# Performance work log

Hardware: AMD Instinct MI355X
Metric: run time of the kernel (lower is better)

## Reference

```python
import jax, jax.numpy as jnp
import numpy as np

B, N = 128, 65536
POS_FRAC = 0.02  # sparse positives, realistic for detection


def setup_inputs() -> dict:
    key = jax.random.key(0)
    k1, k2 = jax.random.split(key)
    pred = jax.random.normal(k1, (B, N), dtype=jnp.float32)
    label = (jax.random.uniform(k2, (B, N)) < POS_FRAC).astype(jnp.float32)
    return {"pred": pred, "label": label}


def _focal_loss_with_mask(pred, label, gamma=2.0, alpha=0.75, negative_ratio=3.0):
    # BCE with logits, elementwise: y*softplus(-x) + (1-y)*softplus(x)
    loss = label * jax.nn.softplus(-pred) + (1.0 - label) * jax.nn.softplus(pred)
    p = jax.nn.sigmoid(pred)
    p_t = label * p + (1.0 - label) * (1.0 - p)
    loss = loss * (1.0 - p_t) ** gamma
    loss = loss * (label * alpha + (1.0 - label) * (1.0 - alpha))

    fn_mask = (p < 0.5) & (label == 1.0)
    fp_mask = (p >= 0.5) & (label == 0.0)

    # --- hard negative mining (vectorized rank-based selection) ---
    pos_mask = label > 0
    num_pos = pos_mask.sum(axis=1, keepdims=True)              # [B,1]
    num_neg = jnp.floor(negative_ratio * num_pos).astype(jnp.int32)  # int() truncation as in torch
    loss_m = jnp.where(pos_mask, -jnp.inf, loss)               # positives sorted last
    order = jnp.argsort(-loss_m, axis=1)                       # descending sort indices
    ranks = jnp.argsort(order, axis=1)                         # rank of each element
    neg_mask = ranks < num_neg
    relevant = pos_mask | neg_mask

    w = alpha / (1.0 - alpha)
    loss = jnp.where(fn_mask | fp_mask, loss * w, loss)
    rm = relevant.astype(loss.dtype)
    return (loss * rm).sum() / rm.sum()


def reference(pred, label):
    return _focal_loss_with_mask(pred, label)
```

## Files before the change

### kernel.cpp

```cpp
#include <hip/hip_runtime.h>
#include <cstdint>
#include <cstddef>

constexpr int B_ROWS = 128;
constexpr int N_COLS = 65536;
constexpr int CAP    = 4096;

constexpr size_t OFF_HISTCNT = 0;
constexpr size_t OFF_CAND    = (size_t)1 << 20;
constexpr size_t OFF_MISC    = (size_t)3 << 20;
constexpr size_t MO_NUMPOS   = 0;
constexpr size_t MO_SPOS     = 512;
constexpr size_t MO_ROWS     = 1024;
constexpr size_t MO_ROWDEN   = 2048;
constexpr size_t MO_CANDBIN  = 2560;
constexpr size_t MO_R1       = 3072;
constexpr size_t MO_KARR     = 3584;
constexpr size_t MO_CANDCNT  = 4096;
constexpr size_t MO_SABOVE   = 4608;
constexpr size_t MO_AUTO64   = 5120;
constexpr size_t MISC_ZERO   = 6144;
constexpr size_t OFF_KEYS    = (size_t)4 << 20;

__device__ __forceinline__ unsigned key_from_pred(float x) {
  unsigned b = __float_as_uint(x);
  return (b & 0x80000000u) ? ~b : (b | 0x80000000u);
}
__device__ __forceinline__ float pred_from_key(unsigned k) {
  unsigned b = (k & 0x80000000u) ? (k ^ 0x80000000u) : ~k;
  return __uint_as_float(b);
}

__device__ __forceinline__ float neg_loss(float x) {
  float ax = fabsf(x);
  float e  = expf(-ax);
  float p  = (x >= 0.0f) ? 1.0f / (1.0f + e) : e / (1.0f + e);
  float sp = fmaxf(x, 0.0f) + log1pf(e);
  float f  = p;
  float l  = sp * f * f * 0.25f;
  return (p >= 0.5f) ? l * 3.0f : l;
}
__device__ __forceinline__ float pos_loss(float x) {
  float ax = fabsf(x);
  float e  = expf(-ax);
  float p  = (x >= 0.0f) ? 1.0f / (1.0f + e) : e / (1.0f + e);
  float sp = fmaxf(-x, 0.0f) + log1pf(e);
  float f  = 1.0f - p;
  float l  = sp * f * f * 0.75f;
  return (p < 0.5f) ? l * 3.0f : l;
}
__device__ __forceinline__ float loss_from_key(unsigned k) { return neg_loss(pred_from_key(k)); }

__device__ void suffix_scan(int* c, float* l, int M) {
  const int T = blockDim.x;
  const int i0 = threadIdx.x, i1 = threadIdx.x + T;
  for (int d = 1; d < M; d <<= 1) {
    int vi0 = 0, vi1 = 0; float vf0 = 0.0f, vf1 = 0.0f;
    const bool h0 = i0 < M, h1 = i1 < M;
    if (h0) { vi0 = c[i0] + ((i0 + d < M) ? c[i0 + d] : 0);
              vf0 = l[i0] + ((i0 + d < M) ? l[i0 + d] : 0.0f); }
    if (h1) { vi1 = c[i1] + ((i1 + d < M) ? c[i1 + d] : 0);
              vf1 = l[i1] + ((i1 + d < M) ? l[i1 + d] : 0.0f); }
    __syncthreads();
    if (h0) { c[i0] = vi0; l[i0] = vf0; }
    if (h1) { c[i1] = vi1; l[i1] = vf1; }
    __syncthreads();
  }
}
__device__ void suffix_scan_i(int* c, int M) {
  const int T = blockDim.x;
  const int i0 = threadIdx.x, i1 = threadIdx.x + T;
  for (int d = 1; d < M; d <<= 1) {
    int v0 = 0, v1 = 0;
    const bool h0 = i0 < M, h1 = i1 < M;
    if (h0) v0 = c[i0] + ((i0 + d < M) ? c[i0 + d] : 0);
    if (h1) v1 = c[i1] + ((i1 + d < M) ? c[i1 + d] : 0);
    __syncthreads();
    if (h0) c[i0] = v0;
    if (h1) c[i1] = v1;
    __syncthreads();
  }
}
__device__ int find_cut(const int* sc, int M, int r, int* ctrl) {
  __syncthreads();
  if (threadIdx.x == 0) *ctrl = -1;
  __syncthreads();
  int loc = -1;
  for (int i = threadIdx.x; i < M; i += blockDim.x)
    if (sc[i] >= r) loc = i;
  if (loc >= 0) atomicMax(ctrl, loc);
  __syncthreads();
  return *ctrl;
}

constexpr int K1_TPB = 256;
constexpr int K1_SEGS = 8;
constexpr int K1_SEG_ELEMS = N_COLS / K1_SEGS;
constexpr int K1_ITERS = K1_SEG_ELEMS / (K1_TPB * 4);

template <bool STORE_KEYS>
__global__ __launch_bounds__(K1_TPB)
void k1_hist(const float* __restrict__ pred, const float* __restrict__ label,
             int* __restrict__ histCnt, int* __restrict__ numPos, float* __restrict__ SPos,
             unsigned* __restrict__ keys)
{
  __shared__ int   hcnt[2048];
  __shared__ int   wnp[K1_TPB / 64];
  __shared__ float wsp[K1_TPB / 64];
  const int tid = threadIdx.x;
  for (int i = tid; i < 2048; i += K1_TPB) hcnt[i] = 0;
  __syncthreads();

  const int row = blockIdx.x / K1_SEGS;
  const int seg = blockIdx.x % K1_SEGS;
  const size_t base = (size_t)row * N_COLS + (size_t)seg * K1_SEG_ELEMS;
  const float4* p4 = reinterpret_cast<const float4*>(pred + base);
  const float4* l4 = reinterpret_cast<const float4*>(label + base);
  uint4* k4 = STORE_KEYS ? reinterpret_cast<uint4*>(keys + base) : nullptr;

  int npos = 0; float spos = 0.0f;
  for (int it = 0; it < K1_ITERS; ++it) {
    const int vi = it * K1_TPB + tid;
    const float4 pv = p4[vi];
    const float4 lv = l4[vi];
    const float xs[4] = {pv.x, pv.y, pv.z, pv.w};
    const float ys[4] = {lv.x, lv.y, lv.z, lv.w};
    unsigned ks[4];
#pragma unroll
    for (int j = 0; j < 4; ++j) {
      const float x = xs[j];
      if (ys[j] > 0.5f) {
        npos += 1;
        spos += pos_loss(x);
        ks[j] = 0u;
      } else {
        const unsigned key = key_from_pred(x);
        ks[j] = key;
        atomicAdd(&hcnt[key >> 21], 1);
      }
    }
    if (STORE_KEYS) { uint4 uk; uk.x = ks[0]; uk.y = ks[1]; uk.z = ks[2]; uk.w = ks[3]; k4[vi] = uk; }
  }

#pragma unroll
  for (int off = 32; off > 0; off >>= 1) {
    npos += __shfl_down(npos, off);
    spos += __shfl_down(spos, off);
  }
  const int wid = tid >> 6, lane = tid & 63;
  if (lane == 0) { wnp[wid] = npos; wsp[wid] = spos; }
  __syncthreads();
  if (tid == 0) {
    int tn = 0; float ts = 0.0f;
    for (int i = 0; i < K1_TPB / 64; ++i) { tn += wnp[i]; ts += wsp[i]; }
    atomicAdd(&numPos[row], tn);
    unsafeAtomicAdd(&SPos[row], ts);
  }
  __syncthreads();
  for (int i = tid; i < 2048; i += K1_TPB)
    if (hcnt[i]) atomicAdd(&histCnt[row * 2048 + i], hcnt[i]);
}

__global__ __launch_bounds__(1024)
void k2a_cut(const int* __restrict__ histCnt, const int* __restrict__ numPos,
             int* __restrict__ candBin, unsigned long long* __restrict__ auto64,
             int* __restrict__ r1Arr, int* __restrict__ kArr)
{
  __shared__ int s_cnt[2048];
  __shared__ int s_ctrl;
  const int tid = threadIdx.x, row = blockIdx.x;
  const int np = numPos[row];
  const int nneg = N_COLS - np;
  const int k = (3 * np < nneg) ? 3 * np : nneg;
  for (int i = tid; i < 2048; i += 1024) s_cnt[i] = histCnt[row * 2048 + i];
  __syncthreads();
  suffix_scan_i(s_cnt, 2048);
  if (k <= 0) {
    if (tid == 0) {
      candBin[row] = -1; auto64[row] = 1ull << 32; r1Arr[row] = 0; kArr[row] = k;
    }
    return;
  }
  const int b1 = find_cut(s_cnt, 2048, k, &s_ctrl);
  if (tid == 0) {
    const int above = (b1 + 1 < 2048) ? s_cnt[b1 + 1] : 0;
    candBin[row] = b1;
    auto64[row]  = (unsigned long long)(b1 + 1) << 21;
    r1Arr[row]   = k - above;
    kArr[row]    = k;
  }
}

constexpr int K2B_TPB = 256;
constexpr int K2B_SEGS = 16;
constexpr int K2B_SEG_ELEMS = N_COLS / K2B_SEGS;
constexpr int K2B_ITERS = K2B_SEG_ELEMS / (K2B_TPB * 4);

template <bool USE_KEYS>
__global__ __launch_bounds__(K2B_TPB)
void k2b_stream(const float* __restrict__ pred, const float* __restrict__ label,
                const unsigned* __restrict__ keys,
                const int* __restrict__ candBin, const unsigned long long* __restrict__ auto64,
                unsigned* __restrict__ candList, int* __restrict__ candCnt,
                float* __restrict__ S_above)
{
  __shared__ unsigned s_cand[K2B_SEG_ELEMS];
  __shared__ int      s_cnt;
  __shared__ int      s_base;
  __shared__ float    wacc[K2B_TPB / 64];

  const int tid = threadIdx.x;
  const int row = blockIdx.x / K2B_SEGS;
  const int seg = blockIdx.x % K2B_SEGS;
  const size_t base = (size_t)row * N_COLS + (size_t)seg * K2B_SEG_ELEMS;
  const int cb = candBin[row];
  const unsigned long long at = auto64[row];
  const int lane = tid & 63, wid = tid >> 6;

  if (tid == 0) s_cnt = 0;
  __syncthreads();

  float acc = 0.0f;
  for (int it = 0; it < K2B_ITERS; ++it) {
    unsigned ks[4];
    if (USE_KEYS) {
      const uint4 kv = reinterpret_cast<const uint4*>(keys + base)[it * K2B_TPB + tid];
      ks[0] = kv.x; ks[1] = kv.y; ks[2] = kv.z; ks[3] = kv.w;
    } else {
      const float4 pv = reinterpret_cast<const float4*>(pred + base)[it * K2B_TPB + tid];
      const float4 lv = reinterpret_cast<const float4*>(label + base)[it * K2B_TPB + tid];
      const float xs[4] = {pv.x, pv.y, pv.z, pv.w};
      const float ys[4] = {lv.x, lv.y, lv.z, lv.w};
#pragma unroll
      for (int j = 0; j < 4; ++j) ks[j] = (ys[j] > 0.5f) ? 0u : key_from_pred(xs[j]);
    }
#pragma unroll
    for (int j = 0; j < 4; ++j) {
      const unsigned key = ks[j];
      if (key == 0u) continue;
      if ((unsigned long long)key >= at) {
        acc += loss_from_key(key);
      } else if ((int)(key >> 21) == cb) {
        const int idx = atomicAdd(&s_cnt, 1);
        s_cand[idx] = key;
      }
    }
  }

#pragma unroll
  for (int off = 32; off > 0; off >>= 1) acc += __shfl_down(acc, off);
  if (lane == 0) wacc[wid] = acc;
  __syncthreads();
  if (tid == 0) {
    float t = 0.0f;
    for (int i = 0; i < K2B_TPB / 64; ++i) t += wacc[i];
    unsafeAtomicAdd(&S_above[row], t);
    s_base = atomicAdd(&candCnt[row], s_cnt);
  }
  __syncthreads();

  const int cnt = s_cnt, gbase = s_base;
  for (int i = tid; i < cnt; i += K2B_TPB) {
    const int g = gbase + i;
    if (g < CAP) candList[(size_t)row * CAP + g] = s_cand[i];
  }
}

template <bool USE_KEYS>
__device__ void stream_bin(const float* __restrict__ pred, const float* __restrict__ label,
                           const unsigned* __restrict__ keys, int row, int b1, int b2,
                           int* hcnt, float* hloss)
{
  const size_t base = (size_t)row * N_COLS;
  const int tid = threadIdx.x;
  for (int it = 0; it < N_COLS / (1024 * 4); ++it) {
    unsigned ks[4];
    if (USE_KEYS) {
      const uint4 kv = reinterpret_cast<const uint4*>(keys + base)[it * 1024 + tid];
      ks[0] = kv.x; ks[1] = kv.y; ks[2] = kv.z; ks[3] = kv.w;
    } else {
      const float4 pv = reinterpret_cast<const float4*>(pred + base)[it * 1024 + tid];
      const float4 lv = reinterpret_cast<const float4*>(label + base)[it * 1024 + tid];
      const float xs[4] = {pv.x, pv.y, pv.z, pv.w};
      const float ys[4] = {lv.x, lv.y, lv.z, lv.w};
#pragma unroll
      for (int j = 0; j < 4; ++j) ks[j] = (ys[j] > 0.5f) ? 0u : key_from_pred(xs[j]);
    }
#pragma unroll
    for (int j = 0; j < 4; ++j) {
      const unsigned key = ks[j];
      if (!key) continue;
      if ((int)(key >> 21) != b1) continue;
      if (b2 < 0) {
        const int b = (key >> 10) & 0x7FF;
        atomicAdd(&hcnt[b], 1);
        atomicAdd(&hloss[b], loss_from_key(key));
      } else {
        if ((int)((key >> 10) & 0x7FF) != b2) continue;
        const int b = key & 0x3FF;
        atomicAdd(&hcnt[b], 1);
        atomicAdd(&hloss[b], loss_from_key(key));
      }
    }
  }
}

template <bool USE_KEYS>
__global__ __launch_bounds__(1024)
void k2c_refine(const float* __restrict__ pred, const float* __restrict__ label,
                const unsigned* __restrict__ keys,
                const int* __restrict__ numPos, const float* __restrict__ SPos,
                const int* __restrict__ candBin, const int* __restrict__ r1Arr,
                const int* __restrict__ kArr, const int* __restrict__ candCnt,
                const unsigned* __restrict__ candList, const float* __restrict__ S_above,
                double* __restrict__ rowS, int* __restrict__ rowDen)
{
  __shared__ unsigned s_key[CAP];
  __shared__ float    s_lv[CAP];
  __shared__ int      h_cnt[2048];
  __shared__ float    h_loss[2048];
  __shared__ int      r3cnt[1024];
  __shared__ float    r3loss[1024];
  __shared__ int      s_ctrl;

  const int tid = threadIdx.x, row = blockIdx.x;
  const int np = numPos[row];
  const int k  = kArr[row];
  if (k <= 0) {
    if (tid == 0) { rowS[row] = (double)SPos[row]; rowDen[row] = np; }
    return;
  }
  const int r1 = r1Arr[row];
  const int b1 = candBin[row];
  const int cc = candCnt[row];
  float S = 0.0f;

  for (int i = tid; i < 2048; i += 1024) { h_cnt[i] = 0; h_loss[i] = 0.0f; }
  __syncthreads();

  int b2, r2;
  if (cc <= CAP) {
    for (int i = tid; i < cc; i += 1024) {
      const unsigned key = candList[(size_t)row * CAP + i];
      const float l = loss_from_key(key);
      s_key[i] = key; s_lv[i] = l;
      const int b = (key >> 10) & 0x7FF;
      atomicAdd(&h_cnt[b], 1);
      atomicAdd(&h_loss[b], l);
    }
    __syncthreads();
    suffix_scan(h_cnt, h_loss, 2048);
    b2 = find_cut(h_cnt, 2048, r1, &s_ctrl);
    r2 = r1 - ((b2 + 1 < 2048) ? h_cnt[b2 + 1] : 0);
    S += (b2 + 1 < 2048) ? h_loss[b2 + 1] : 0.0f;
    __syncthreads();

    for (int i = tid; i < 1024; i += 1024) { r3cnt[i] = 0; r3loss[i] = 0.0f; }
    __syncthreads();
    for (int i = tid; i < cc; i += 1024) {
      const unsigned key = s_key[i];
      if ((int)((key >> 10) & 0x7FF) == b2) {
        atomicAdd(&r3cnt[key & 0x3FF], 1);
        atomicAdd(&r3loss[key & 0x3FF], s_lv[i]);
      }
    }
    __syncthreads();
  } else {
    stream_bin<USE_KEYS>(pred, label, keys, row, b1, -1, h_cnt, h_loss);
    __syncthreads();
    suffix_scan(h_cnt, h_loss, 2048);
    b2 = find_cut(h_cnt, 2048, r1, &s_ctrl);
    r2 = r1 - ((b2 + 1 < 2048) ? h_cnt[b2 + 1] : 0);
    S += (b2 + 1 < 2048) ? h_loss[b2 + 1] : 0.0f;
    __syncthreads();
    for (int i = tid; i < 1024; i += 1024) { r3cnt[i] = 0; r3loss[i] = 0.0f; }
    __syncthreads();
    stream_bin<USE_KEYS>(pred, label, keys, row, b1, b2, r3cnt, r3loss);
    __syncthreads();
  }

  for (int i = tid; i < 1024; i += 1024) { h_cnt[i] = r3cnt[i]; h_loss[i] = r3loss[i]; }
  __syncthreads();
  suffix_scan(h_cnt, h_loss, 1024);
  const int b3 = find_cut(h_cnt, 1024, r2, &s_ctrl);
  const int r3 = r2 - ((b3 + 1 < 1024) ? h_cnt[b3 + 1] : 0);
  S += (b3 + 1 < 1024) ? h_loss[b3 + 1] : 0.0f;
  S += (float)r3 * (r3loss[b3] / (float)r3cnt[b3]);

  if (tid == 0) {
    rowS[row] = (double)S + (double)S_above[row] + (double)SPos[row];
    rowDen[row] = np + k;
  }
}

__global__ __launch_bounds__(B_ROWS)
void k3_final(const double* __restrict__ rowS, const int* __restrict__ rowDen,
              float* __restrict__ out)
{
  __shared__ double sd[B_ROWS];
  __shared__ long long si[B_ROWS];
  const int t = threadIdx.x;
  sd[t] = rowS[t];
  si[t] = (long long)rowDen[t];
  __syncthreads();
  if (t == 0) {
    double s = 0.0; long long d = 0;
    for (int i = 0; i < B_ROWS; ++i) { s += sd[i]; d += si[i]; }
    out[0] = (float)(s / (double)d);
  }
}

extern "C" void kernel_launch(void* const* d_in, const int* in_sizes, int n_in,
                              void* d_out, int out_size, void* d_ws, size_t ws_size,
                              hipStream_t stream)
{
  const float* pred  = (const float*)d_in[0];
  const float* label = (const float*)d_in[1];
  float* out = (float*)d_out;
  char* ws = (char*)d_ws;

  int*      histCnt = (int*)(ws + OFF_HISTCNT);
  unsigned* cand    = (unsigned*)(ws + OFF_CAND);
  char*     misc    = ws + OFF_MISC;
  int*      numPos  = (int*)(misc + MO_NUMPOS);
  float*    SPos    = (float*)(misc + MO_SPOS);
  double*   rowS    = (double*)(misc + MO_ROWS);
  int*      rowDen  = (int*)(misc + MO_ROWDEN);
  int*      candBin = (int*)(misc + MO_CANDBIN);
  int*      r1Arr   = (int*)(misc + MO_R1);
  int*      kArr    = (int*)(misc + MO_KARR);
  int*      candCnt = (int*)(misc + MO_CANDCNT);
  float*    S_above = (float*)(misc + MO_SABOVE);
  unsigned long long* auto64 = (unsigned long long*)(misc + MO_AUTO64);
  unsigned* keys    = (unsigned*)(ws + OFF_KEYS);

  const bool useKeys = ws_size >= OFF_KEYS + (size_t)B_ROWS * N_COLS * sizeof(unsigned);

  hipMemsetAsync(ws + OFF_HISTCNT, 0, (size_t)1 << 20, stream);
  hipMemsetAsync(ws + OFF_MISC, 0, MISC_ZERO, stream);

  const dim3 g1(B_ROWS * K1_SEGS), t1(K1_TPB);
  const dim3 g2a(B_ROWS), t2a(1024);
  const dim3 g2b(B_ROWS * K2B_SEGS), t2b(K2B_TPB);
  const dim3 g2c(B_ROWS), t2c(1024);

  if (useKeys) {
    k1_hist<true><<<g1, t1, 0, stream>>>(pred, label, histCnt, numPos, SPos, keys);
    k2a_cut<<<g2a, t2a, 0, stream>>>(histCnt, numPos, candBin, auto64, r1Arr, kArr);
    k2b_stream<true><<<g2b, t2b, 0, stream>>>(pred, label, keys, candBin, auto64, cand, candCnt, S_above);
    k2c_refine<true><<<g2c, t2c, 0, stream>>>(pred, label, keys, numPos, SPos, candBin, r1Arr, kArr,
                                              candCnt, cand, S_above, rowS, rowDen);
  } else {
    k1_hist<false><<<g1, t1, 0, stream>>>(pred, label, histCnt, numPos, SPos, nullptr);
    k2a_cut<<<g2a, t2a, 0, stream>>>(histCnt, numPos, candBin, auto64, r1Arr, kArr);
    k2b_stream<false><<<g2b, t2b, 0, stream>>>(pred, label, nullptr, candBin, auto64, cand, candCnt, S_above);
    k2c_refine<false><<<g2c, t2c, 0, stream>>>(pred, label, nullptr, numPos, SPos, candBin, r1Arr, kArr,
                                               candCnt, cand, S_above, rowS, rowDen);
  }
  k3_final<<<dim3(1), dim3(B_ROWS), 0, stream>>>(rowS, rowDen, out);
}
```

Measured before the change: 175.8 us.

## Replace global histogram atomics with per-slab writes and fold final reduction

k1 now writes each block's 2048-bin histogram and positive stats to its own slab instead of atomically accumulating into per-row buffers. k2a sums the eight slabs per row and zeroes the downstream accumulators itself, so both memsets go away. The final k3 kernel is replaced by a last-block-done atomic reduction inside k2c. This cuts two memset launches and one kernel launch plus global atomic traffic, at the cost of 8MB of extra slab writes and reads and a larger workspace footprint.

```diff
diff --git a/kernel.cpp b/kernel.cpp
--- a/kernel.cpp
+++ b/kernel.cpp
@@ -6,21 +6,23 @@
 constexpr int N_COLS = 65536;
 constexpr int CAP    = 4096;
 
-constexpr size_t OFF_HISTCNT = 0;
-constexpr size_t OFF_CAND    = (size_t)1 << 20;
-constexpr size_t OFF_MISC    = (size_t)3 << 20;
+constexpr size_t OFF_SLABCNT = 0;
+constexpr size_t OFF_SLABNP  = (size_t)8 << 20;
+constexpr size_t OFF_SLABSP  = ((size_t)8 << 20) + 4096;
+constexpr size_t OFF_CAND    = (size_t)9 << 20;
+constexpr size_t OFF_MISC    = (size_t)12 << 20;
 constexpr size_t MO_NUMPOS   = 0;
 constexpr size_t MO_SPOS     = 512;
-constexpr size_t MO_ROWS     = 1024;
-constexpr size_t MO_ROWDEN   = 2048;
-constexpr size_t MO_CANDBIN  = 2560;
-constexpr size_t MO_R1       = 3072;
-constexpr size_t MO_KARR     = 3584;
-constexpr size_t MO_CANDCNT  = 4096;
-constexpr size_t MO_SABOVE   = 4608;
-constexpr size_t MO_AUTO64   = 5120;
-constexpr size_t MISC_ZERO   = 6144;
-constexpr size_t OFF_KEYS    = (size_t)4 << 20;
+constexpr size_t MO_CANDBIN  = 1024;
+constexpr size_t MO_R1       = 1536;
+constexpr size_t MO_KARR     = 2048;
+constexpr size_t MO_CANDCNT  = 2560;
+constexpr size_t MO_SABOVE   = 3072;
+constexpr size_t MO_AUTO64   = 3584;
+constexpr size_t MO_GNUM     = 4608;
+constexpr size_t MO_GDEN     = 4616;
+constexpr size_t MO_GDONE    = 4620;
+constexpr size_t OFF_KEYS    = (size_t)16 << 20;
 
 __device__ __forceinline__ unsigned key_from_pred(float x) {
   unsigned b = __float_as_uint(x);
@@ -101,7 +103,7 @@
 template <bool STORE_KEYS>
 __global__ __launch_bounds__(K1_TPB)
 void k1_hist(const float* __restrict__ pred, const float* __restrict__ label,
-             int* __restrict__ histCnt, int* __restrict__ numPos, float* __restrict__ SPos,
+             int* __restrict__ slabCnt, int* __restrict__ slabNP, float* __restrict__ slabSP,
              unsigned* __restrict__ keys)
 {
   __shared__ int   hcnt[2048];
@@ -111,9 +113,8 @@
   for (int i = tid; i < 2048; i += K1_TPB) hcnt[i] = 0;
   __syncthreads();
 
-  const int row = blockIdx.x / K1_SEGS;
-  const int seg = blockIdx.x % K1_SEGS;
-  const size_t base = (size_t)row * N_COLS + (size_t)seg * K1_SEG_ELEMS;
+  const int blk = blockIdx.x;
+  const size_t base = (size_t)blk * K1_SEG_ELEMS;
   const float4* p4 = reinterpret_cast<const float4*>(pred + base);
   const float4* l4 = reinterpret_cast<const float4*>(label + base);
   uint4* k4 = STORE_KEYS ? reinterpret_cast<uint4*>(keys + base) : nullptr;
@@ -153,42 +154,67 @@
   if (tid == 0) {
     int tn = 0; float ts = 0.0f;
     for (int i = 0; i < K1_TPB / 64; ++i) { tn += wnp[i]; ts += wsp[i]; }
-    atomicAdd(&numPos[row], tn);
-    unsafeAtomicAdd(&SPos[row], ts);
-  }
-  __syncthreads();
+    slabNP[blk] = tn;
+    slabSP[blk] = ts;
+  }
   for (int i = tid; i < 2048; i += K1_TPB)
-    if (hcnt[i]) atomicAdd(&histCnt[row * 2048 + i], hcnt[i]);
+    slabCnt[(size_t)blk * 2048 + i] = hcnt[i];
 }
 
 __global__ __launch_bounds__(1024)
-void k2a_cut(const int* __restrict__ histCnt, const int* __restrict__ numPos,
+void k2a_cut(const int* __restrict__ slabCnt, const int* __restrict__ slabNP,
+             const float* __restrict__ slabSP,
+             int* __restrict__ numPos, float* __restrict__ SPos,
              int* __restrict__ candBin, unsigned long long* __restrict__ auto64,
-             int* __restrict__ r1Arr, int* __restrict__ kArr)
+             int* __restrict__ r1Arr, int* __restrict__ kArr,
+             int* __restrict__ candCnt, float* __restrict__ S_above,
+             double* __restrict__ gNum, int* __restrict__ gDen, int* __restrict__ gDone)
 {
   __shared__ int s_cnt[2048];
   __shared__ int s_ctrl;
+  __shared__ int s_np;
+  __shared__ float s_sp;
   const int tid = threadIdx.x, row = blockIdx.x;
-  const int np = numPos[row];
+
+  if (tid == 0) {
+    int tn = 0; float ts = 0.0f;
+    for (int s = 0; s < K1_SEGS; ++s) { tn += slabNP[row * K1_SEGS + s]; ts += slabSP[row * K1_SEGS + s]; }
+    s_np = tn; s_sp = ts;
+  }
+  for (int i = tid; i < 2048; i += 1024) {
+    int v = 0;
+#pragma unroll
+    for (int s = 0; s < K1_SEGS; ++s) v += slabCnt[((size_t)(row * K1_SEGS + s)) * 2048 + i];
+    s_cnt[i] = v;
+  }
+  __syncthreads();
+
+  const int np = s_np;
   const int nneg = N_COLS - np;
   const int k = (3 * np < nneg) ? 3 * np : nneg;
-  for (int i = tid; i < 2048; i += 1024) s_cnt[i] = histCnt[row * 2048 + i];
-  __syncthreads();
+
   suffix_scan_i(s_cnt, 2048);
-  if (k <= 0) {
-    if (tid == 0) {
-      candBin[row] = -1; auto64[row] = 1ull << 32; r1Arr[row] = 0; kArr[row] = k;
-    }
-    return;
-  }
-  const int b1 = find_cut(s_cnt, 2048, k, &s_ctrl);
+  int b1 = -1;
+  if (k > 0) b1 = find_cut(s_cnt, 2048, k, &s_ctrl);
+
   if (tid == 0) {
-    const int above = (b1 + 1 < 2048) ? s_cnt[b1 + 1] : 0;
-    candBin[row] = b1;
-    auto64[row]  = (unsigned long long)(b1 + 1) << 21;
-    r1Arr[row]   = k - above;
+    numPos[row]  = np;
+    SPos[row]    = s_sp;
+    candCnt[row] = 0;
+    S_above[row] = 0.0f;
     kArr[row]    = k;
-  }
+    if (k > 0) {
+      const int above = (b1 + 1 < 2048) ? s_cnt[b1 + 1] : 0;
+      candBin[row] = b1;
+      auto64[row]  = (unsigned long long)(b1 + 1) << 21;
+      r1Arr[row]   = k - above;
+    } else {
+      candBin[row] = -1;
+      auto64[row]  = 1ull << 32;
+      r1Arr[row]   = 0;
+    }
+  }
+  if (row == 0 && tid == 1) { *gNum = 0.0; *gDen = 0; *gDone = 0; }
 }
 
 constexpr int K2B_TPB = 256;
@@ -313,7 +339,8 @@
                 const int* __restrict__ candBin, const int* __restrict__ r1Arr,
                 const int* __restrict__ kArr, const int* __restrict__ candCnt,
                 const unsigned* __restrict__ candList, const float* __restrict__ S_above,
-                double* __restrict__ rowS, int* __restrict__ rowDen)
+                double* __restrict__ gNum, int* __restrict__ gDen, int* __restrict__ gDone,
+                float* __restrict__ out)
 {
   __shared__ unsigned s_key[CAP];
   __shared__ float    s_lv[CAP];
@@ -326,87 +353,79 @@
   const int tid = threadIdx.x, row = blockIdx.x;
   const int np = numPos[row];
   const int k  = kArr[row];
-  if (k <= 0) {
-    if (tid == 0) { rowS[row] = (double)SPos[row]; rowDen[row] = np; }
-    return;
-  }
-  const int r1 = r1Arr[row];
-  const int b1 = candBin[row];
-  const int cc = candCnt[row];
   float S = 0.0f;
 
-  for (int i = tid; i < 2048; i += 1024) { h_cnt[i] = 0; h_loss[i] = 0.0f; }
-  __syncthreads();
-
-  int b2, r2;
-  if (cc <= CAP) {
-    for (int i = tid; i < cc; i += 1024) {
-      const unsigned key = candList[(size_t)row * CAP + i];
-      const float l = loss_from_key(key);
-      s_key[i] = key; s_lv[i] = l;
-      const int b = (key >> 10) & 0x7FF;
-      atomicAdd(&h_cnt[b], 1);
-      atomicAdd(&h_loss[b], l);
-    }
-    __syncthreads();
-    suffix_scan(h_cnt, h_loss, 2048);
-    b2 = find_cut(h_cnt, 2048, r1, &s_ctrl);
-    r2 = r1 - ((b2 + 1 < 2048) ? h_cnt[b2 + 1] : 0);
-    S += (b2 + 1 < 2048) ? h_loss[b2 + 1] : 0.0f;
-    __syncthreads();
-
-    for (int i = tid; i < 1024; i += 1024) { r3cnt[i] = 0; r3loss[i] = 0.0f; }
-    __syncthreads();
-    for (int i = tid; i < cc; i += 1024) {
-      const unsigned key = s_key[i];
-      if ((int)((key >> 10) & 0x7FF) == b2) {
-        atomicAdd(&r3cnt[key & 0x3FF], 1);
-        atomicAdd(&r3loss[key & 0x3FF], s_lv[i]);
+  if (k > 0) {
+    const int r1 = r1Arr[row];
+    const int b1 = candBin[row];
+    const int cc = candCnt[row];
+
+    for (int i = tid; i < 2048; i += 1024) { h_cnt[i] = 0; h_loss[i] = 0.0f; }
+    __syncthreads();
+
+    int b2, r2;
+    if (cc <= CAP) {
+      for (int i = tid; i < cc; i += 1024) {
+        const unsigned key = candList[(size_t)row * CAP + i];
+        const float l = loss_from_key(key);
+        s_key[i] = key; s_lv[i] = l;
+        const int b = (key >> 10) & 0x7FF;
+        atomicAdd(&h_cnt[b], 1);
+        atomicAdd(&h_loss[b], l);
       }
-    }
-    __syncthreads();
-  } else {
-    stream_bin<USE_KEYS>(pred, label, keys, row, b1, -1, h_cnt, h_loss);
-    __syncthreads();
-    suffix_scan(h_cnt, h_loss, 2048);
-    b2 = find_cut(h_cnt, 2048, r1, &s_ctrl);
-    r2 = r1 - ((b2 + 1 < 2048) ? h_cnt[b2 + 1] : 0);
-    S += (b2 + 1 < 2048) ? h_loss[b2 + 1] : 0.0f;
-    __syncthreads();
-    for (int i = tid; i < 1024; i += 1024) { r3cnt[i] = 0; r3loss[i] = 0.0f; }
-    __syncthreads();
-    stream_bin<USE_KEYS>(pred, label, keys, row, b1, b2, r3cnt, r3loss);
-    __syncthreads();
-  }
-
-  for (int i = tid; i < 1024; i += 1024) { h_cnt[i] = r3cnt[i]; h_loss[i] = r3loss[i]; }
-  __syncthreads();
-  suffix_scan(h_cnt, h_loss, 1024);
-  const int b3 = find_cut(h_cnt, 1024, r2, &s_ctrl);
-  const int r3 = r2 - ((b3 + 1 < 1024) ? h_cnt[b3 + 1] : 0);
-  S += (b3 + 1 < 1024) ? h_loss[b3 + 1] : 0.0f;
-  S += (float)r3 * (r3loss[b3] / (float)r3cnt[b3]);
+      __syncthreads();
+      suffix_scan(h_cnt, h_loss, 2048);
+      b2 = find_cut(h_cnt, 2048, r1, &s_ctrl);
+      r2 = r1 - ((b2 + 1 < 2048) ? h_cnt[b2 + 1] : 0);
+      S += (b2 + 1 < 2048) ? h_loss[b2 + 1] : 0.0f;
+      __syncthreads();
+
+      for (int i = tid; i < 1024; i += 1024) { r3cnt[i] = 0; r3loss[i] = 0.0f; }
+      __syncthreads();
+      for (int i = tid; i < cc; i += 1024) {
+        const unsigned key = s_key[i];
+        if ((int)((key >> 10) & 0x7FF) == b2) {
+          atomicAdd(&r3cnt[key & 0x3FF], 1);
+          atomicAdd(&r3loss[key & 0x3FF], s_lv[i]);
+        }
+      }
+      __syncthreads();
+    } else {
+      stream_bin<USE_KEYS>(pred, label, keys, row, b1, -1, h_cnt, h_loss);
+      __syncthreads();
+      suffix_scan(h_cnt, h_loss, 2048);
+      b2 = find_cut(h_cnt, 2048, r1, &s_ctrl);
+      r2 = r1 - ((b2 + 1 < 2048) ? h_cnt[b2 + 1] : 0);
+      S += (b2 + 1 < 2048) ? h_loss[b2 + 1] : 0.0f;
+      __syncthreads();
+      for (int i = tid; i < 1024; i += 1024) { r3cnt[i] = 0; r3loss[i] = 0.0f; }
+      __syncthreads();
+      stream_bin<USE_KEYS>(pred, label, keys, row, b1, b2, r3cnt, r3loss);
+      __syncthreads();
+    }
+
+    for (int i = tid; i < 1024; i += 1024) { h_cnt[i] = r3cnt[i]; h_loss[i] = r3loss[i]; }
+    __syncthreads();
+    suffix_scan(h_cnt, h_loss, 1024);
+    const int b3 = find_cut(h_cnt, 1024, r2, &s_ctrl);
+    const int r3 = r2 - ((b3 + 1 < 1024) ? h_cnt[b3 + 1] : 0);
+    S += (b3 + 1 < 1024) ? h_loss[b3 + 1] : 0.0f;
+    S += (float)r3 * (r3loss[b3] / (float)r3cnt[b3]);
+  }
 
   if (tid == 0) {
-    rowS[row] = (double)S + (double)S_above[row] + (double)SPos[row];
-    rowDen[row] = np + k;
-  }
-}
-
-__global__ __launch_bounds__(B_ROWS)
-void k3_final(const double* __restrict__ rowS, const int* __restrict__ rowDen,
-              float* __restrict__ out)
-{
-  __shared__ double sd[B_ROWS];
-  __shared__ long long si[B_ROWS];
-  const int t = threadIdx.x;
-  sd[t] = rowS[t];
-  si[t] = (long long)rowDen[t];
-  __syncthreads();
-  if (t == 0) {
-    double s = 0.0; long long d = 0;
-    for (int i = 0; i < B_ROWS; ++i) { s += sd[i]; d += si[i]; }
-    out[0] = (float)(s / (double)d);
+    const double contrib = (double)SPos[row] +
+                           (k > 0 ? (double)S + (double)S_above[row] : 0.0);
+    const int dcontrib = np + (k > 0 ? k : 0);
+    unsafeAtomicAdd(gNum, contrib);
+    atomicAdd(gDen, dcontrib);
+    __threadfence();
+    const int old = atomicAdd(gDone, 1);
+    if (old == B_ROWS - 1) {
+      const double num = unsafeAtomicAdd(gNum, 0.0);
+      const int    den = atomicAdd(gDen, 0);
+      out[0] = (float)(num / (double)den);
+    }
   }
 }
 
@@ -419,25 +438,25 @@
   float* out = (float*)d_out;
   char* ws = (char*)d_ws;
 
-  int*      histCnt = (int*)(ws + OFF_HISTCNT);
+  int*      slabCnt = (int*)(ws + OFF_SLABCNT);
+  int*      slabNP  = (int*)(ws + OFF_SLABNP);
+  float*    slabSP  = (float*)(ws + OFF_SLABSP);
   unsigned* cand    = (unsigned*)(ws + OFF_CAND);
   char*     misc    = ws + OFF_MISC;
   int*      numPos  = (int*)(misc + MO_NUMPOS);
   float*    SPos    = (float*)(misc + MO_SPOS);
-  double*   rowS    = (double*)(misc + MO_ROWS);
-  int*      rowDen  = (int*)(misc + MO_ROWDEN);
   int*      candBin = (int*)(misc + MO_CANDBIN);
   int*      r1Arr   = (int*)(misc + MO_R1);
   int*      kArr    = (int*)(misc + MO_KARR);
   int*      candCnt = (int*)(misc + MO_CANDCNT);
   float*    S_above = (float*)(misc + MO_SABOVE);
   unsigned long long* auto64 = (unsigned long long*)(misc + MO_AUTO64);
+  double*   gNum    = (double*)(misc + MO_GNUM);
+  int*      gDen    = (int*)(misc + MO_GDEN);
+  int*      gDone   = (int*)(misc + MO_GDONE);
   unsigned* keys    = (unsigned*)(ws + OFF_KEYS);
 
   const bool useKeys = ws_size >= OFF_KEYS + (size_t)B_ROWS * N_COLS * sizeof(unsigned);
-
-  hipMemsetAsync(ws + OFF_HISTCNT, 0, (size_t)1 << 20, stream);
-  hipMemsetAsync(ws + OFF_MISC, 0, MISC_ZERO, stream);
 
   const dim3 g1(B_ROWS * K1_SEGS), t1(K1_TPB);
   const dim3 g2a(B_ROWS), t2a(1024);
@@ -445,17 +464,18 @@
   const dim3 g2c(B_ROWS), t2c(1024);
 
   if (useKeys) {
-    k1_hist<true><<<g1, t1, 0, stream>>>(pred, label, histCnt, numPos, SPos, keys);
-    k2a_cut<<<g2a, t2a, 0, stream>>>(histCnt, numPos, candBin, auto64, r1Arr, kArr);
+    k1_hist<true><<<g1, t1, 0, stream>>>(pred, label, slabCnt, slabNP, slabSP, keys);
+    k2a_cut<<<g2a, t2a, 0, stream>>>(slabCnt, slabNP, slabSP, numPos, SPos, candBin, auto64,
+                                     r1Arr, kArr, candCnt, S_above, gNum, gDen, gDone);
     k2b_stream<true><<<g2b, t2b, 0, stream>>>(pred, label, keys, candBin, auto64, cand, candCnt, S_above);
     k2c_refine<true><<<g2c, t2c, 0, stream>>>(pred, label, keys, numPos, SPos, candBin, r1Arr, kArr,
-                                              candCnt, cand, S_above, rowS, rowDen);
+                                              candCnt, cand, S_above, gNum, gDen, gDone, out);
   } else {
-    k1_hist<false><<<g1, t1, 0, stream>>>(pred, label, histCnt, numPos, SPos, nullptr);
-    k2a_cut<<<g2a, t2a, 0, stream>>>(histCnt, numPos, candBin, auto64, r1Arr, kArr);
+    k1_hist<false><<<g1, t1, 0, stream>>>(pred, label, slabCnt, slabNP, slabSP, nullptr);
+    k2a_cut<<<g2a, t2a, 0, stream>>>(slabCnt, slabNP, slabSP, numPos, SPos, candBin, auto64,
+                                     r1Arr, kArr, candCnt, S_above, gNum, gDen, gDone);
     k2b_stream<false><<<g2b, t2b, 0, stream>>>(pred, label, nullptr, candBin, auto64, cand, candCnt, S_above);
     k2c_refine<false><<<g2c, t2c, 0, stream>>>(pred, label, nullptr, numPos, SPos, candBin, r1Arr, kArr,
-                                               candCnt, cand, S_above, rowS, rowDen);
-  }
-  k3_final<<<dim3(1), dim3(B_ROWS), 0, stream>>>(rowS, rowDen, out);
-}
+                                               candCnt, cand, S_above, gNum, gDen, gDone, out);
+  }
+}
```

After: 175.9 us. About the same (+0.0%).
